# Optimization experiments

Hardware: AMD Instinct MI355X
Metric: run time of the kernel (lower is better)

Reference implementation:

```python
import jax, jax.numpy as jnp
import numpy as np

N_NODES = 100000
N_EDGES = 3200000
F_IN, F_HID, F_OUT = 512, 16, 64


def gcn_conv(x, src, dst, W, b, n):
    # Linear transform first (PyG GCNConv: x @ W, then normalized aggregation, then + bias)
    xw = x @ W  # [n, f_out]
    # symmetric normalization with self-loops (gcn_norm, improved=False)
    deg = jax.ops.segment_sum(jnp.ones_like(dst, dtype=xw.dtype), dst, num_segments=n)
    deg_inv_sqrt = jnp.where(deg > 0, jax.lax.rsqrt(jnp.maximum(deg, 1e-12)), 0.0)
    norm = deg_inv_sqrt[src] * deg_inv_sqrt[dst]  # [E+n]
    out = jax.ops.segment_sum(norm[:, None] * xw[src], dst, num_segments=n)
    return out + b


def setup_inputs() -> dict:
    key = jax.random.key(0)
    k1, k2, k3, k4, k5, k6 = jax.random.split(key, 6)
    x = jax.random.normal(k1, (N_NODES, F_IN), dtype=jnp.float32)
    edge_index = jax.random.randint(k2, (2, N_EDGES), 0, N_NODES, dtype=jnp.int64)
    # Glorot init like PyG GCNConv
    s1 = (6.0 / (F_IN + F_HID)) ** 0.5
    s2 = (6.0 / (F_HID + F_OUT)) ** 0.5
    W1 = jax.random.uniform(k3, (F_IN, F_HID), jnp.float32, -s1, s1)
    b1 = jnp.zeros((F_HID,), jnp.float32)
    W2 = jax.random.uniform(k4, (F_HID, F_OUT), jnp.float32, -s2, s2)
    b2 = jnp.zeros((F_OUT,), jnp.float32)
    return {"x": x, "edge_index": edge_index, "W1": W1, "b1": b1, "W2": W2, "b2": b2}


def reference(x, edge_index, W1, b1, W2, b2):
    n = x.shape[0]
    loop = jnp.arange(n, dtype=edge_index.dtype)
    src = jnp.concatenate([edge_index[0], loop])
    dst = jnp.concatenate([edge_index[1], loop])
    h = jax.nn.relu(gcn_conv(x, src, dst, W1, b1, n))
    out = jax.nn.relu(gcn_conv(h, src, dst, W2, b2, n))
    return out
```

## Files before the change

kernel.cpp:

```cpp
#include <hip/hip_runtime.h>

constexpr int NN   = 100000;
constexpr int NE   = 3200000;
constexpr int FIN  = 512;
constexpr int FH   = 16;
constexpr int FOUT = 64;

constexpr int BSH = 6;
constexpr int BSZ = 64;
constexpr int K   = (NN + BSZ - 1) / BSZ;
constexpr int NB  = 512;
constexpr int CHUNK = NE / NB;
constexpr int CAP = 4096;

constexpr int G1B = 1024;
constexpr int G1T = 128;
constexpr int NPB = 98;

__global__ __launch_bounds__(256) void k_cnt(const int* __restrict__ ei, int* __restrict__ M) {
    __shared__ int h[K];
    int t = threadIdx.x, b = blockIdx.x;
    for (int i = t; i < K; i += 256) h[i] = 0;
    __syncthreads();
    int e0 = b * CHUNK;
    for (int e = e0 + t; e < e0 + CHUNK; e += 256)
        atomicAdd(&h[ei[NE + e] >> BSH], 1);
    __syncthreads();
    for (int i = t; i < K; i += 256) M[i * NB + b] = h[i];
}

__global__ __launch_bounds__(256) void k_scanM(int* __restrict__ M, int* __restrict__ btot) {
    int k = blockIdx.x, t = threadIdx.x;
    int2* row = (int2*)(M + (size_t)k * NB);
    int2 v = row[t];
    int s = v.x + v.y;
    int lane = t & 63, wid = t >> 6;
    int ps = s;
    #pragma unroll
    for (int off = 1; off < 64; off <<= 1) {
        int u = __shfl_up(ps, off, 64);
        if (lane >= off) ps += u;
    }
    __shared__ int wsum[4];
    if (lane == 63) wsum[wid] = ps;
    __syncthreads();
    int base = 0;
    for (int w = 0; w < wid; ++w) base += wsum[w];
    int excl = base + ps - s;
    int2 o; o.x = excl; o.y = excl + v.x;
    row[t] = o;
    if (t == 255) btot[k] = excl + s;
}

__global__ __launch_bounds__(1024) void k_scanB(const int* __restrict__ btot, int* __restrict__ bstart) {
    int t = threadIdx.x;
    int i0 = 2 * t, i1 = 2 * t + 1;
    int c0 = (i0 < K) ? btot[i0] : 0;
    int c1 = (i1 < K) ? btot[i1] : 0;
    int s = c0 + c1;
    int lane = t & 63, wid = t >> 6;
    int ps = s;
    #pragma unroll
    for (int off = 1; off < 64; off <<= 1) {
        int u = __shfl_up(ps, off, 64);
        if (lane >= off) ps += u;
    }
    __shared__ int wsum[16];
    if (lane == 63) wsum[wid] = ps;
    __syncthreads();
    int base = 0;
    for (int w = 0; w < wid; ++w) base += wsum[w];
    int excl = base + ps - s;
    if (i0 < K) bstart[i0] = excl;
    if (i1 < K) bstart[i1] = excl + c0;
    if (t == 0) bstart[K] = NE;
}

__global__ __launch_bounds__(256) void k_scatter2(const int* __restrict__ ei,
                                                  const int* __restrict__ M,
                                                  const int* __restrict__ bstart,
                                                  int* __restrict__ rec) {
    __shared__ int cur[K];
    int t = threadIdx.x, b = blockIdx.x;
    for (int i = t; i < K; i += 256) cur[i] = bstart[i] + M[i * NB + b];
    __syncthreads();
    int e0 = b * CHUNK;
    for (int e = e0 + t; e < e0 + CHUNK; e += 256) {
        int s = ei[e];
        int d = ei[NE + e];
        int pos = atomicAdd(&cur[d >> BSH], 1);
        rec[pos] = (s << BSH) | (d & (BSZ - 1));
    }
}

__global__ __launch_bounds__(256) void k_sort2(const int* __restrict__ rec1,
                                               const int* __restrict__ bstart,
                                               int* __restrict__ rec2,
                                               int* __restrict__ row_ptr,
                                               float* __restrict__ dis) {
    __shared__ int h[BSZ];
    __shared__ int cur[BSZ];
    int t = threadIdx.x, k = blockIdx.x;
    if (t < BSZ) h[t] = 0;
    __syncthreads();
    int e0 = bstart[k], e1 = bstart[k + 1];
    for (int e = e0 + t; e < e1; e += 256)
        atomicAdd(&h[rec1[e] & (BSZ - 1)], 1);
    __syncthreads();
    if (t < BSZ) {
        int c = h[t];
        int ps = c;
        #pragma unroll
        for (int off = 1; off < 64; off <<= 1) {
            int u = __shfl_up(ps, off, 64);
            if (t >= off) ps += u;
        }
        int excl = ps - c;
        cur[t] = excl;
        int node = k * BSZ + t;
        if (node < NN) {
            row_ptr[node] = e0 + excl;
            dis[node] = rsqrtf((float)c + 1.0f);
        }
    }
    __syncthreads();
    for (int e = e0 + t; e < e1; e += 256) {
        int r = rec1[e];
        int pos = atomicAdd(&cur[r & (BSZ - 1)], 1);
        rec2[e0 + pos] = r >> BSH;
    }
    if (k == 0 && t == 0) row_ptr[NN] = NE;
}

__device__ __forceinline__ void cons16(float acc[FH], float4 a0, float4 a1, float4 a2, float4 a3,
                                       const float* __restrict__ wrow) {
    float xs[16] = {a0.x, a0.y, a0.z, a0.w, a1.x, a1.y, a1.z, a1.w,
                    a2.x, a2.y, a2.z, a2.w, a3.x, a3.y, a3.z, a3.w};
    #pragma unroll
    for (int c = 0; c < 16; ++c) {
        float xv = xs[c];
        const float* w = &wrow[c * FH];
        #pragma unroll
        for (int jb = 0; jb < 4; ++jb) {
            float4 wv = *(const float4*)&w[jb * 4];
            acc[jb * 4 + 0] += xv * wv.x;
            acc[jb * 4 + 1] += xv * wv.y;
            acc[jb * 4 + 2] += xv * wv.z;
            acc[jb * 4 + 3] += xv * wv.w;
        }
    }
}

__global__ __launch_bounds__(G1T) void k_gemm1(const float* __restrict__ x,
                                               const float* __restrict__ W1,
                                               const float* __restrict__ dis,
                                               float* __restrict__ vp1) {
    __shared__ float ws[FIN * FH];
    int t = threadIdx.x;
    #pragma unroll
    for (int i = 0; i < 16; ++i)
        *(float4*)&ws[i * 512 + t * 4] = *(const float4*)&W1[i * 512 + t * 4];
    int node = blockIdx.x * NPB + t;
    bool live = (t < NPB) && (node < NN);
    int n = live ? node : NN - 1;
    const float* xr = x + (size_t)n * FIN;
    float acc[FH];
    #pragma unroll
    for (int j = 0; j < FH; ++j) acc[j] = 0.f;
    float4 A0 = *(const float4*)&xr[0],  A1 = *(const float4*)&xr[4],
           A2 = *(const float4*)&xr[8],  A3 = *(const float4*)&xr[12];
    float4 B0 = *(const float4*)&xr[16], B1 = *(const float4*)&xr[20],
           B2 = *(const float4*)&xr[24], B3 = *(const float4*)&xr[28];
    __syncthreads();
    #pragma unroll 1
    for (int k0 = 0; k0 + 48 <= FIN; k0 += 32) {
        float4 C0 = *(const float4*)&xr[k0 + 32], C1 = *(const float4*)&xr[k0 + 36],
               C2 = *(const float4*)&xr[k0 + 40], C3 = *(const float4*)&xr[k0 + 44];
        cons16(acc, A0, A1, A2, A3, &ws[k0 * FH]);
        A0 = C0; A1 = C1; A2 = C2; A3 = C3;
        float4 D0 = *(const float4*)&xr[k0 + 48], D1 = *(const float4*)&xr[k0 + 52],
               D2 = *(const float4*)&xr[k0 + 56], D3 = *(const float4*)&xr[k0 + 60];
        cons16(acc, B0, B1, B2, B3, &ws[(k0 + 16) * FH]);
        B0 = D0; B1 = D1; B2 = D2; B3 = D3;
    }
    cons16(acc, A0, A1, A2, A3, &ws[(FIN - 32) * FH]);
    cons16(acc, B0, B1, B2, B3, &ws[(FIN - 16) * FH]);
    if (live) {
        float dv = dis[node];
        #pragma unroll
        for (int jb = 0; jb < 4; ++jb)
            *(float4*)&vp1[(size_t)node * FH + jb * 4] =
                make_float4(dv * acc[jb * 4], dv * acc[jb * 4 + 1],
                            dv * acc[jb * 4 + 2], dv * acc[jb * 4 + 3]);
    }
}

__device__ __forceinline__ float4 seg_gather(const int* __restrict__ recs,
                                             const int* __restrict__ gsrc,
                                             int a, int b, int nst,
                                             const float* __restrict__ vp, int q) {
    float4 acc = make_float4(0.f, 0.f, 0.f, 0.f);
    int blds = b < nst ? b : nst;
    int i = a;
    for (; i + 8 <= blds; i += 8) {
        int r0 = recs[i],     r1 = recs[i + 1], r2 = recs[i + 2], r3 = recs[i + 3];
        int r4 = recs[i + 4], r5 = recs[i + 5], r6 = recs[i + 6], r7 = recs[i + 7];
        float4 v0 = *(const float4*)&vp[(size_t)r0 * FH + q * 4];
        float4 v1 = *(const float4*)&vp[(size_t)r1 * FH + q * 4];
        float4 v2 = *(const float4*)&vp[(size_t)r2 * FH + q * 4];
        float4 v3 = *(const float4*)&vp[(size_t)r3 * FH + q * 4];
        float4 v4 = *(const float4*)&vp[(size_t)r4 * FH + q * 4];
        float4 v5 = *(const float4*)&vp[(size_t)r5 * FH + q * 4];
        float4 v6 = *(const float4*)&vp[(size_t)r6 * FH + q * 4];
        float4 v7 = *(const float4*)&vp[(size_t)r7 * FH + q * 4];
        acc.x += ((v0.x + v1.x) + (v2.x + v3.x)) + ((v4.x + v5.x) + (v6.x + v7.x));
        acc.y += ((v0.y + v1.y) + (v2.y + v3.y)) + ((v4.y + v5.y) + (v6.y + v7.y));
        acc.z += ((v0.z + v1.z) + (v2.z + v3.z)) + ((v4.z + v5.z) + (v6.z + v7.z));
        acc.w += ((v0.w + v1.w) + (v2.w + v3.w)) + ((v4.w + v5.w) + (v6.w + v7.w));
    }
    for (; i < blds; ++i) {
        int r0 = recs[i];
        float4 v0 = *(const float4*)&vp[(size_t)r0 * FH + q * 4];
        acc.x += v0.x; acc.y += v0.y; acc.z += v0.z; acc.w += v0.w;
    }
    for (int j = (a > nst ? a : nst); j < b; ++j) {
        int r0 = gsrc[j];
        float4 v0 = *(const float4*)&vp[(size_t)r0 * FH + q * 4];
        acc.x += v0.x; acc.y += v0.y; acc.z += v0.z; acc.w += v0.w;
    }
    return acc;
}

__global__ __launch_bounds__(256) void k_agg1(const int* __restrict__ rec2,
                                              const int* __restrict__ bstart,
                                              const int* __restrict__ row_ptr,
                                              const float* __restrict__ dis,
                                              const float* __restrict__ vp1,
                                              const float* __restrict__ b1,
                                              float* __restrict__ vp2) {
    __shared__ int recs[CAP];
    int t = threadIdx.x, k = blockIdx.x;
    int e0 = bstart[k], e1 = bstart[k + 1];
    int len = e1 - e0, nst = len < CAP ? len : CAP;
    for (int i = t; i < nst; i += 256) recs[i] = rec2[e0 + i];
    __syncthreads();
    int slot = t >> 2, q = t & 3;
    int node = k * BSZ + slot;
    if (node >= NN) return;
    int a = row_ptr[node] - e0;
    int b = row_ptr[node + 1] - e0;
    float4 acc = seg_gather(recs, rec2 + e0, a, b, nst, vp1, q);
    float dv = dis[node];
    float4 self = *(const float4*)&vp1[(size_t)node * FH + q * 4];
    float4 bb   = *(const float4*)&b1[q * 4];
    float4 o;
    o.x = dv * fmaxf(dv * (acc.x + self.x) + bb.x, 0.f);
    o.y = dv * fmaxf(dv * (acc.y + self.y) + bb.y, 0.f);
    o.z = dv * fmaxf(dv * (acc.z + self.z) + bb.z, 0.f);
    o.w = dv * fmaxf(dv * (acc.w + self.w) + bb.w, 0.f);
    *(float4*)&vp2[(size_t)node * FH + q * 4] = o;
}

__global__ __launch_bounds__(256) void k_agg2(const int* __restrict__ rec2,
                                              const int* __restrict__ bstart,
                                              const int* __restrict__ row_ptr,
                                              const float* __restrict__ dis,
                                              const float* __restrict__ vp2,
                                              const float* __restrict__ W2,
                                              const float* __restrict__ b2,
                                              float* __restrict__ out) {
    __shared__ int   recs[CAP];
    __shared__ float a16[BSZ * FH];
    __shared__ float ws[FH * FOUT];
    int t = threadIdx.x, k = blockIdx.x;
    *(float4*)&ws[t * 4] = *(const float4*)&W2[t * 4];
    int e0 = bstart[k], e1 = bstart[k + 1];
    int len = e1 - e0, nst = len < CAP ? len : CAP;
    for (int i = t; i < nst; i += 256) recs[i] = rec2[e0 + i];
    __syncthreads();
    int slot = t >> 2, q = t & 3;
    int node = k * BSZ + slot;
    float4 r = make_float4(0.f, 0.f, 0.f, 0.f);
    if (node < NN) {
        int a = row_ptr[node] - e0;
        int b = row_ptr[node + 1] - e0;
        float4 acc = seg_gather(recs, rec2 + e0, a, b, nst, vp2, q);
        float dv = dis[node];
        float4 self = *(const float4*)&vp2[(size_t)node * FH + q * 4];
        r.x = dv * (acc.x + self.x);
        r.y = dv * (acc.y + self.y);
        r.z = dv * (acc.z + self.z);
        r.w = dv * (acc.w + self.w);
    }
    *(float4*)&a16[slot * FH + q * 4] = r;
    __syncthreads();
    int j = t & 63;
    float bj = b2[j];
    float wreg[FH];
    #pragma unroll
    for (int kk = 0; kk < FH; ++kk) wreg[kk] = ws[kk * FOUT + j];
    for (int n = t >> 6; n < BSZ; n += 4) {
        int node2 = k * BSZ + n;
        if (node2 >= NN) break;
        const float* ar = &a16[n * FH];
        float s = 0.f;
        #pragma unroll
        for (int kk = 0; kk < FH; ++kk) s += ar[kk] * wreg[kk];
        out[(size_t)node2 * FOUT + j] = fmaxf(s + bj, 0.f);
    }
}

extern "C" void kernel_launch(void* const* d_in, const int* in_sizes, int n_in,
                              void* d_out, int out_size, void* d_ws, size_t ws_size,
                              hipStream_t stream) {
    const float* x  = (const float*)d_in[0];
    const int*   ei = (const int*)d_in[1];
    const float* W1 = (const float*)d_in[2];
    const float* b1 = (const float*)d_in[3];
    const float* W2 = (const float*)d_in[4];
    const float* b2 = (const float*)d_in[5];
    float* out = (float*)d_out;

    char* p = (char*)d_ws;
    int*   M       = (int*)p;    p += (size_t)K * NB * 4;
    int*   btot    = (int*)p;    p += 2048 * 4;
    int*   bstart  = (int*)p;    p += 2048 * 4;
    char*  bufA    = p;          p += (size_t)NE * 4;
    int*   rec2    = (int*)p;    p += (size_t)NE * 4;
    int*   row_ptr = (int*)p;    p += 100032 * 4;
    float* dis     = (float*)p;  p += 100032 * 4;

    int*   rec1 = (int*)bufA;
    float* vp1  = (float*)bufA;
    float* vp2  = (float*)(bufA + (size_t)NN * FH * 4);

    k_cnt     <<<NB, 256, 0, stream>>>(ei, M);
    k_scanM   <<<K, 256, 0, stream>>>(M, btot);
    k_scanB   <<<1, 1024, 0, stream>>>(btot, bstart);
    k_scatter2<<<NB, 256, 0, stream>>>(ei, M, bstart, rec1);
    k_sort2   <<<K, 256, 0, stream>>>(rec1, bstart, rec2, row_ptr, dis);

    k_gemm1   <<<G1B, G1T, 0, stream>>>(x, W1, dis, vp1);
    k_agg1    <<<K, 256, 0, stream>>>(rec2, bstart, row_ptr, dis, vp1, b1, vp2);
    k_agg2    <<<K, 256, 0, stream>>>(rec2, bstart, row_ptr, dis, vp2, W2, b2, out);
}
```

Before: 481.0 us.

## Use coarse 1024-node buckets for two-pass counting sort of edges

The first radix pass now buckets edges by dst>>10 (98 buckets) instead of dst>>6 (1563 buckets). This shrinks the per-block histogram and the M matrix, cuts scan work, and replaces scattered writes into many buckets with fewer, larger streams. The second pass sorts within each 1024-node bucket using a 1024-entry shared histogram and a block-wide scan. The aggregation kernels now derive edge ranges from row_ptr instead of bstart. The trade-off is only 98 blocks in the second sort pass, which may underuse the GPU's compute units, and more shared-memory atomic contention per block.

```diff
diff --git a/kernel.cpp b/kernel.cpp
--- a/kernel.cpp
+++ b/kernel.cpp
@@ -6,30 +6,32 @@
 constexpr int FH   = 16;
 constexpr int FOUT = 64;
 
-constexpr int BSH = 6;
-constexpr int BSZ = 64;
-constexpr int K   = (NN + BSZ - 1) / BSZ;
-constexpr int NB  = 512;
+constexpr int BSZ  = 64;
+constexpr int KAGG = (NN + BSZ - 1) / BSZ;
+constexpr int NB   = 512;
 constexpr int CHUNK = NE / NB;
-constexpr int CAP = 4096;
+constexpr int CAP  = 4096;
+
+constexpr int BKB  = 10;
+constexpr int NBK  = (NN + 1023) >> 10;
 
 constexpr int G1B = 1024;
 constexpr int G1T = 128;
 constexpr int NPB = 98;
 
-__global__ __launch_bounds__(256) void k_cnt(const int* __restrict__ ei, int* __restrict__ M) {
-    __shared__ int h[K];
+__global__ __launch_bounds__(256) void k_cntA(const int* __restrict__ ei, int* __restrict__ M) {
+    __shared__ int h[NBK];
     int t = threadIdx.x, b = blockIdx.x;
-    for (int i = t; i < K; i += 256) h[i] = 0;
+    if (t < NBK) h[t] = 0;
     __syncthreads();
     int e0 = b * CHUNK;
     for (int e = e0 + t; e < e0 + CHUNK; e += 256)
-        atomicAdd(&h[ei[NE + e] >> BSH], 1);
-    __syncthreads();
-    for (int i = t; i < K; i += 256) M[i * NB + b] = h[i];
-}
-
-__global__ __launch_bounds__(256) void k_scanM(int* __restrict__ M, int* __restrict__ btot) {
+        atomicAdd(&h[ei[NE + e] >> BKB], 1);
+    __syncthreads();
+    if (t < NBK) M[t * NB + b] = h[t];
+}
+
+__global__ __launch_bounds__(256) void k_scanA(int* __restrict__ M, int* __restrict__ btot) {
     int k = blockIdx.x, t = threadIdx.x;
     int2* row = (int2*)(M + (size_t)k * NB);
     int2 v = row[t];
@@ -52,82 +54,90 @@
     if (t == 255) btot[k] = excl + s;
 }
 
-__global__ __launch_bounds__(1024) void k_scanB(const int* __restrict__ btot, int* __restrict__ bstart) {
+__global__ __launch_bounds__(64) void k_scanBA(const int* __restrict__ btot, int* __restrict__ bstartA) {
     int t = threadIdx.x;
     int i0 = 2 * t, i1 = 2 * t + 1;
-    int c0 = (i0 < K) ? btot[i0] : 0;
-    int c1 = (i1 < K) ? btot[i1] : 0;
+    int c0 = (i0 < NBK) ? btot[i0] : 0;
+    int c1 = (i1 < NBK) ? btot[i1] : 0;
     int s = c0 + c1;
-    int lane = t & 63, wid = t >> 6;
     int ps = s;
     #pragma unroll
     for (int off = 1; off < 64; off <<= 1) {
         int u = __shfl_up(ps, off, 64);
-        if (lane >= off) ps += u;
-    }
-    __shared__ int wsum[16];
-    if (lane == 63) wsum[wid] = ps;
-    __syncthreads();
-    int base = 0;
-    for (int w = 0; w < wid; ++w) base += wsum[w];
-    int excl = base + ps - s;
-    if (i0 < K) bstart[i0] = excl;
-    if (i1 < K) bstart[i1] = excl + c0;
-    if (t == 0) bstart[K] = NE;
-}
-
-__global__ __launch_bounds__(256) void k_scatter2(const int* __restrict__ ei,
-                                                  const int* __restrict__ M,
-                                                  const int* __restrict__ bstart,
-                                                  int* __restrict__ rec) {
-    __shared__ int cur[K];
+        if (t >= off) ps += u;
+    }
+    int excl = ps - s;
+    if (i0 < NBK) bstartA[i0] = excl;
+    if (i1 < NBK) bstartA[i1] = excl + c0;
+    if (t == 0) bstartA[NBK] = NE;
+}
+
+__global__ __launch_bounds__(256) void k_scatA(const int* __restrict__ ei,
+                                               const int* __restrict__ M,
+                                               const int* __restrict__ bstartA,
+                                               int* __restrict__ rec1) {
+    __shared__ int cur[NBK];
     int t = threadIdx.x, b = blockIdx.x;
-    for (int i = t; i < K; i += 256) cur[i] = bstart[i] + M[i * NB + b];
+    if (t < NBK) cur[t] = bstartA[t] + M[t * NB + b];
     __syncthreads();
     int e0 = b * CHUNK;
     for (int e = e0 + t; e < e0 + CHUNK; e += 256) {
         int s = ei[e];
         int d = ei[NE + e];
-        int pos = atomicAdd(&cur[d >> BSH], 1);
-        rec[pos] = (s << BSH) | (d & (BSZ - 1));
-    }
-}
-
-__global__ __launch_bounds__(256) void k_sort2(const int* __restrict__ rec1,
-                                               const int* __restrict__ bstart,
+        int pos = atomicAdd(&cur[d >> BKB], 1);
+        rec1[pos] = (s << BKB) | (d & 1023);
+    }
+}
+
+__global__ __launch_bounds__(256) void k_sortA(const int* __restrict__ rec1,
+                                               const int* __restrict__ bstartA,
                                                int* __restrict__ rec2,
                                                int* __restrict__ row_ptr,
                                                float* __restrict__ dis) {
-    __shared__ int h[BSZ];
-    __shared__ int cur[BSZ];
+    __shared__ int h[1024];
+    __shared__ int cur[1024];
+    __shared__ int wsum[4];
     int t = threadIdx.x, k = blockIdx.x;
-    if (t < BSZ) h[t] = 0;
-    __syncthreads();
-    int e0 = bstart[k], e1 = bstart[k + 1];
+    *(int4*)&h[4 * t] = make_int4(0, 0, 0, 0);
+    __syncthreads();
+    int e0 = bstartA[k], e1 = bstartA[k + 1];
     for (int e = e0 + t; e < e1; e += 256)
-        atomicAdd(&h[rec1[e] & (BSZ - 1)], 1);
-    __syncthreads();
-    if (t < BSZ) {
-        int c = h[t];
-        int ps = c;
+        atomicAdd(&h[rec1[e] & 1023], 1);
+    __syncthreads();
+    int i0 = 4 * t;
+    int c0 = h[i0], c1 = h[i0 + 1], c2 = h[i0 + 2], c3 = h[i0 + 3];
+    int s = c0 + c1 + c2 + c3;
+    int lane = t & 63, wid = t >> 6;
+    int ps = s;
+    #pragma unroll
+    for (int off = 1; off < 64; off <<= 1) {
+        int u = __shfl_up(ps, off, 64);
+        if (lane >= off) ps += u;
+    }
+    if (lane == 63) wsum[wid] = ps;
+    __syncthreads();
+    int base = 0;
+    for (int w = 0; w < wid; ++w) base += wsum[w];
+    int ex = base + ps - s;
+    int e0x = ex, e1x = ex + c0, e2x = e1x + c1, e3x = e2x + c2;
+    cur[i0] = e0x; cur[i0 + 1] = e1x; cur[i0 + 2] = e2x; cur[i0 + 3] = e3x;
+    int node = (k << BKB) + i0;
+    if (node + 3 < NN) {
+        *(int4*)&row_ptr[node] = make_int4(e0 + e0x, e0 + e1x, e0 + e2x, e0 + e3x);
+        *(float4*)&dis[node]   = make_float4(rsqrtf((float)c0 + 1.f), rsqrtf((float)c1 + 1.f),
+                                             rsqrtf((float)c2 + 1.f), rsqrtf((float)c3 + 1.f));
+    } else {
+        int exs[4] = {e0x, e1x, e2x, e3x};
+        int cs[4]  = {c0, c1, c2, c3};
         #pragma unroll
-        for (int off = 1; off < 64; off <<= 1) {
-            int u = __shfl_up(ps, off, 64);
-            if (t >= off) ps += u;
-        }
-        int excl = ps - c;
-        cur[t] = excl;
-        int node = k * BSZ + t;
-        if (node < NN) {
-            row_ptr[node] = e0 + excl;
-            dis[node] = rsqrtf((float)c + 1.0f);
-        }
+        for (int j = 0; j < 4; ++j)
+            if (node + j < NN) { row_ptr[node + j] = e0 + exs[j]; dis[node + j] = rsqrtf((float)cs[j] + 1.f); }
     }
     __syncthreads();
     for (int e = e0 + t; e < e1; e += 256) {
         int r = rec1[e];
-        int pos = atomicAdd(&cur[r & (BSZ - 1)], 1);
-        rec2[e0 + pos] = r >> BSH;
+        int pos = atomicAdd(&cur[r & 1023], 1);
+        rec2[e0 + pos] = r >> BKB;
     }
     if (k == 0 && t == 0) row_ptr[NN] = NE;
 }
@@ -232,7 +242,6 @@
 }
 
 __global__ __launch_bounds__(256) void k_agg1(const int* __restrict__ rec2,
-                                              const int* __restrict__ bstart,
                                               const int* __restrict__ row_ptr,
                                               const float* __restrict__ dis,
                                               const float* __restrict__ vp1,
@@ -240,12 +249,14 @@
                                               float* __restrict__ vp2) {
     __shared__ int recs[CAP];
     int t = threadIdx.x, k = blockIdx.x;
-    int e0 = bstart[k], e1 = bstart[k + 1];
+    int n0 = k * BSZ;
+    int nend = n0 + BSZ < NN ? n0 + BSZ : NN;
+    int e0 = row_ptr[n0], e1 = row_ptr[nend];
     int len = e1 - e0, nst = len < CAP ? len : CAP;
     for (int i = t; i < nst; i += 256) recs[i] = rec2[e0 + i];
     __syncthreads();
     int slot = t >> 2, q = t & 3;
-    int node = k * BSZ + slot;
+    int node = n0 + slot;
     if (node >= NN) return;
     int a = row_ptr[node] - e0;
     int b = row_ptr[node + 1] - e0;
@@ -262,7 +273,6 @@
 }
 
 __global__ __launch_bounds__(256) void k_agg2(const int* __restrict__ rec2,
-                                              const int* __restrict__ bstart,
                                               const int* __restrict__ row_ptr,
                                               const float* __restrict__ dis,
                                               const float* __restrict__ vp2,
@@ -274,12 +284,14 @@
     __shared__ float ws[FH * FOUT];
     int t = threadIdx.x, k = blockIdx.x;
     *(float4*)&ws[t * 4] = *(const float4*)&W2[t * 4];
-    int e0 = bstart[k], e1 = bstart[k + 1];
+    int n0 = k * BSZ;
+    int nend = n0 + BSZ < NN ? n0 + BSZ : NN;
+    int e0 = row_ptr[n0], e1 = row_ptr[nend];
     int len = e1 - e0, nst = len < CAP ? len : CAP;
     for (int i = t; i < nst; i += 256) recs[i] = rec2[e0 + i];
     __syncthreads();
     int slot = t >> 2, q = t & 3;
-    int node = k * BSZ + slot;
+    int node = n0 + slot;
     float4 r = make_float4(0.f, 0.f, 0.f, 0.f);
     if (node < NN) {
         int a = row_ptr[node] - e0;
@@ -300,7 +312,7 @@
     #pragma unroll
     for (int kk = 0; kk < FH; ++kk) wreg[kk] = ws[kk * FOUT + j];
     for (int n = t >> 6; n < BSZ; n += 4) {
-        int node2 = k * BSZ + n;
+        int node2 = n0 + n;
         if (node2 >= NN) break;
         const float* ar = &a16[n * FH];
         float s = 0.f;
@@ -322,25 +334,25 @@
     float* out = (float*)d_out;
 
     char* p = (char*)d_ws;
-    int*   M       = (int*)p;    p += (size_t)K * NB * 4;
-    int*   btot    = (int*)p;    p += 2048 * 4;
-    int*   bstart  = (int*)p;    p += 2048 * 4;
+    int*   M       = (int*)p;    p += (size_t)NBK * NB * 4;
+    int*   btot    = (int*)p;    p += 128 * 4;
+    int*   bstartA = (int*)p;    p += 128 * 4;
     char*  bufA    = p;          p += (size_t)NE * 4;
     int*   rec2    = (int*)p;    p += (size_t)NE * 4;
-    int*   row_ptr = (int*)p;    p += 100032 * 4;
-    float* dis     = (float*)p;  p += 100032 * 4;
+    int*   row_ptr = (int*)p;    p += 100368 * 4;
+    float* dis     = (float*)p;  p += 100368 * 4;
 
     int*   rec1 = (int*)bufA;
     float* vp1  = (float*)bufA;
     float* vp2  = (float*)(bufA + (size_t)NN * FH * 4);
 
-    k_cnt     <<<NB, 256, 0, stream>>>(ei, M);
-    k_scanM   <<<K, 256, 0, stream>>>(M, btot);
-    k_scanB   <<<1, 1024, 0, stream>>>(btot, bstart);
-    k_scatter2<<<NB, 256, 0, stream>>>(ei, M, bstart, rec1);
-    k_sort2   <<<K, 256, 0, stream>>>(rec1, bstart, rec2, row_ptr, dis);
-
-    k_gemm1   <<<G1B, G1T, 0, stream>>>(x, W1, dis, vp1);
-    k_agg1    <<<K, 256, 0, stream>>>(rec2, bstart, row_ptr, dis, vp1, b1, vp2);
-    k_agg2    <<<K, 256, 0, stream>>>(rec2, bstart, row_ptr, dis, vp2, W2, b2, out);
-}
+    k_cntA  <<<NB,  256, 0, stream>>>(ei, M);
+    k_scanA <<<NBK, 256, 0, stream>>>(M, btot);
+    k_scanBA<<<1,   64,  0, stream>>>(btot, bstartA);
+    k_scatA <<<NB,  256, 0, stream>>>(ei, M, bstartA, rec1);
+    k_sortA <<<NBK, 256, 0, stream>>>(rec1, bstartA, rec2, row_ptr, dis);
+
+    k_gemm1 <<<G1B, G1T, 0, stream>>>(x, W1, dis, vp1);
+    k_agg1  <<<KAGG, 256, 0, stream>>>(rec2, row_ptr, dis, vp1, b1, vp2);
+    k_agg2  <<<KAGG, 256, 0, stream>>>(rec2, row_ptr, dis, vp2, W2, b2, out);
+}
```

After: 501.6 us. 1.04x slower.
